# Performance work log

Measured on AMD Instinct MI355X. Metric: run time of the kernel, lower is better.

The kernel has to match this reference:

```python
import jax, jax.numpy as jnp
import numpy as np

B, N, E, H = 2, 4096, 512, 8
D = E // H  # head size


def setup_inputs() -> dict:
    key = jax.random.key(0)
    ks = jax.random.split(key, 11)
    s = 1.0 / np.sqrt(E)
    inp = {
        'q': jax.random.normal(ks[0], (B, N, E), jnp.float32),
        'k': jax.random.normal(ks[1], (B, N, E), jnp.float32),
        'v': jax.random.normal(ks[2], (B, N, E), jnp.float32),
        'Wq': jax.random.uniform(ks[3], (E, E), jnp.float32, -s, s),
        'bq': jax.random.uniform(ks[4], (E,), jnp.float32, -s, s),
        'Wk': jax.random.uniform(ks[5], (E, E), jnp.float32, -s, s),
        'bk': jax.random.uniform(ks[6], (E,), jnp.float32, -s, s),
        'Wv': jax.random.uniform(ks[7], (E, E), jnp.float32, -s, s),
        'bv': jax.random.uniform(ks[8], (E,), jnp.float32, -s, s),
        'Wo': jax.random.uniform(ks[9], (E, E), jnp.float32, -s, s),
        'bo': jax.random.uniform(ks[10], (E,), jnp.float32, -s, s),
    }
    return inp


def reference(q, k, v, Wq, bq, Wk, bk, Wv, bv, Wo, bo):
    # Linear projections (torch Linear: x @ W.T + b)
    qp = (q @ Wq.T + bq).reshape(B, N, H, D).transpose(0, 2, 1, 3)  # [B,H,N,D]
    kp = (k @ Wk.T + bk).reshape(B, N, H, D).transpose(0, 2, 1, 3)
    vp = (v @ Wv.T + bv).reshape(B, N, H, D).transpose(0, 2, 1, 3)
    scores = jnp.einsum('bhnd,bhmd->bhnm', qp, kp) / jnp.sqrt(jnp.float32(D))
    attn = jax.nn.softmax(scores, axis=-1)
    out = jnp.einsum('bhnm,bhmd->bhnd', attn, vp)  # [B,H,N,D]
    out = out.transpose(0, 2, 1, 3).reshape(B, N, E)
    return out @ Wo.T + bo
```

## Files before the change

### kernel.cpp

```cpp
#include <hip/hip_runtime.h>
#include <hip/hip_bf16.h>
#include <cstddef>
#include <cstdint>


typedef __bf16 bf16_t;
typedef __bf16 bf16x8 __attribute__((ext_vector_type(8)));
typedef __bf16 bf16x4 __attribute__((ext_vector_type(4)));
typedef float  f32x4  __attribute__((ext_vector_type(4)));

#define MFMA_BF16 __builtin_amdgcn_mfma_f32_16x16x32_bf16

static __device__ __forceinline__ bf16x8 cvt2(const float4& a, const float4& b) {
  return bf16x8{(bf16_t)a.x,(bf16_t)a.y,(bf16_t)a.z,(bf16_t)a.w,
                (bf16_t)b.x,(bf16_t)b.y,(bf16_t)b.z,(bf16_t)b.w};
}

static __device__ __forceinline__ uint32_t pk2(float a, float b) {
  uint32_t r;
  asm("v_cvt_pk_bf16_f32 %0, %1, %2" : "=v"(r) : "v"(a), "v"(b));
  return r;
}

__global__ void __launch_bounds__(256, 2)
qkv_proj(const float* __restrict__ q, const float* __restrict__ k,
         const float* __restrict__ v,
         const float* __restrict__ Wq, const float* __restrict__ bq,
         const float* __restrict__ Wk, const float* __restrict__ bk,
         const float* __restrict__ Wv, const float* __restrict__ bv,
         bf16_t* __restrict__ Qp, bf16_t* __restrict__ Kp,
         bf16_t* __restrict__ Vt, float qscale)
{
  __shared__ __align__(16) bf16_t As[2][128 * 72];
  __shared__ __align__(16) bf16_t Bs[2][128 * 72];
  const int l     = blockIdx.x;
  const int slice = l >> 8;
  const int inner = l & 255;
  const int mtile = ((inner >> 5) << 3) | (inner & 7);
  const int ntile = (inner >> 3) & 3;
  const int tid   = threadIdx.x;
  const int w     = tid >> 6;
  const int lane  = tid & 63;
  const int lr    = lane & 15;
  const int quad  = lane >> 4;
  const int wm    = w & 1;
  const int wn    = w >> 1;
  const int xrow  = tid >> 1, xcol = (tid & 1) << 5;

  const float* Xf   = (slice == 0) ? q  : (slice == 1) ? k  : v;
  const float* W    = (slice == 0) ? Wq : (slice == 1) ? Wk : Wv;
  const float* bias = (slice == 0) ? bq : (slice == 1) ? bk : bv;
  const float scale = (slice == 0) ? qscale : 1.0f;

  float bvv[4];
#pragma unroll
  for (int ci = 0; ci < 4; ++ci) bvv[ci] = bias[ntile * 128 + wn * 64 + ci * 16 + lr];

  f32x4 acc[4][4] = {};
  float4 xa[8], wa[8];

#pragma unroll
  for (int j = 0; j < 4; ++j) {
    const float* p = Xf + (size_t)(mtile * 128 + xrow) * 512 + xcol + j * 8;
    xa[2*j]   = *(const float4*)p;
    xa[2*j+1] = *(const float4*)(p + 4);
    const float* pw = W + (size_t)(ntile * 128 + xrow) * 512 + xcol + j * 8;
    wa[2*j]   = *(const float4*)pw;
    wa[2*j+1] = *(const float4*)(pw + 4);
  }
#pragma unroll
  for (int j = 0; j < 4; ++j) {
    *(bf16x8*)(&As[0][xrow * 72 + xcol + j * 8]) = cvt2(xa[2*j], xa[2*j+1]);
    *(bf16x8*)(&Bs[0][xrow * 72 + xcol + j * 8]) = cvt2(wa[2*j], wa[2*j+1]);
  }
  __syncthreads();

  for (int it = 0; it < 8; ++it) {
    const int cur = it & 1, nxt = cur ^ 1;
    if (it != 7) {
      const int k0 = (it + 1) << 6;
#pragma unroll
      for (int j = 0; j < 4; ++j) {
        const float* p = Xf + (size_t)(mtile * 128 + xrow) * 512 + k0 + xcol + j * 8;
        xa[2*j]   = *(const float4*)p;
        xa[2*j+1] = *(const float4*)(p + 4);
        const float* pw = W + (size_t)(ntile * 128 + xrow) * 512 + k0 + xcol + j * 8;
        wa[2*j]   = *(const float4*)pw;
        wa[2*j+1] = *(const float4*)(pw + 4);
      }
    }
    bf16x8 af[4][2], bfr[4][2];
#pragma unroll
    for (int mi = 0; mi < 4; ++mi)
#pragma unroll
      for (int kh = 0; kh < 2; ++kh)
        af[mi][kh] = *(const bf16x8*)(&As[cur][(wm * 64 + mi * 16 + lr) * 72 + (kh * 4 + quad) * 8]);
#pragma unroll
    for (int ci = 0; ci < 4; ++ci)
#pragma unroll
      for (int kh = 0; kh < 2; ++kh)
        bfr[ci][kh] = *(const bf16x8*)(&Bs[cur][(wn * 64 + ci * 16 + lr) * 72 + (kh * 4 + quad) * 8]);
#pragma unroll
    for (int mi = 0; mi < 4; ++mi)
#pragma unroll
      for (int ci = 0; ci < 4; ++ci) {
        acc[mi][ci] = MFMA_BF16(af[mi][0], bfr[ci][0], acc[mi][ci], 0, 0, 0);
        acc[mi][ci] = MFMA_BF16(af[mi][1], bfr[ci][1], acc[mi][ci], 0, 0, 0);
      }
    if (it != 7) {
#pragma unroll
      for (int j = 0; j < 4; ++j) {
        *(bf16x8*)(&As[nxt][xrow * 72 + xcol + j * 8]) = cvt2(xa[2*j], xa[2*j+1]);
        *(bf16x8*)(&Bs[nxt][xrow * 72 + xcol + j * 8]) = cvt2(wa[2*j], wa[2*j+1]);
      }
    }
    __syncthreads();
  }

  bf16_t* outQK = (slice == 0) ? Qp : Kp;
#pragma unroll
  for (int mi = 0; mi < 4; ++mi) {
    const int gm0 = mtile * 128 + wm * 64 + mi * 16 + quad * 4;
#pragma unroll
    for (int ci = 0; ci < 4; ++ci) {
      const int gc = ntile * 128 + wn * 64 + ci * 16 + lr;
      const int h = gc >> 6, dd = gc & 63;
      if (slice < 2) {
#pragma unroll
        for (int r = 0; r < 4; ++r) {
          const int gm = gm0 + r;
          const int b = gm >> 12, n = gm & 4095;
          outQK[(size_t)((b * 8 + h) * 4096 + n) * 64 + dd] =
              (bf16_t)((acc[mi][ci][r] + bvv[ci]) * scale);
        }
      } else {
        const int b = gm0 >> 12, n0 = gm0 & 4095;
        bf16x4 pk;
#pragma unroll
        for (int r = 0; r < 4; ++r) pk[r] = (bf16_t)(acc[mi][ci][r] + bvv[ci]);
        *(bf16x4*)(Vt + (size_t)((b * 8 + h) * 64 + dd) * 4096 + n0) = pk;
      }
    }
  }
}

__global__ void __launch_bounds__(256, 2)
o_proj(const bf16_t* __restrict__ Xb, const float* __restrict__ W,
       const float* __restrict__ bias, float* __restrict__ out)
{
  __shared__ __align__(16) bf16_t As[2][128 * 72];
  __shared__ __align__(16) bf16_t Bs[2][128 * 72];
  const int l     = blockIdx.x;
  const int mtile = ((l >> 5) << 3) | (l & 7);
  const int ntile = (l >> 3) & 3;
  const int tid   = threadIdx.x;
  const int w     = tid >> 6;
  const int lane  = tid & 63;
  const int lr    = lane & 15;
  const int quad  = lane >> 4;
  const int wm    = w & 1;
  const int wn    = w >> 1;
  const int xrow  = tid >> 1, xcol = (tid & 1) << 5;

  float bvv[4];
#pragma unroll
  for (int ci = 0; ci < 4; ++ci) bvv[ci] = bias[ntile * 128 + wn * 64 + ci * 16 + lr];

  f32x4 acc[4][4] = {};
  float4 wa[8];
  bf16x8 xb[4];

#pragma unroll
  for (int j = 0; j < 4; ++j) {
    xb[j] = *(const bf16x8*)(Xb + (size_t)(mtile * 128 + xrow) * 512 + xcol + j * 8);
    const float* pw = W + (size_t)(ntile * 128 + xrow) * 512 + xcol + j * 8;
    wa[2*j]   = *(const float4*)pw;
    wa[2*j+1] = *(const float4*)(pw + 4);
  }
#pragma unroll
  for (int j = 0; j < 4; ++j) {
    *(bf16x8*)(&As[0][xrow * 72 + xcol + j * 8]) = xb[j];
    *(bf16x8*)(&Bs[0][xrow * 72 + xcol + j * 8]) = cvt2(wa[2*j], wa[2*j+1]);
  }
  __syncthreads();

  for (int it = 0; it < 8; ++it) {
    const int cur = it & 1, nxt = cur ^ 1;
    if (it != 7) {
      const int k0 = (it + 1) << 6;
#pragma unroll
      for (int j = 0; j < 4; ++j) {
        xb[j] = *(const bf16x8*)(Xb + (size_t)(mtile * 128 + xrow) * 512 + k0 + xcol + j * 8);
        const float* pw = W + (size_t)(ntile * 128 + xrow) * 512 + k0 + xcol + j * 8;
        wa[2*j]   = *(const float4*)pw;
        wa[2*j+1] = *(const float4*)(pw + 4);
      }
    }
    bf16x8 af[4][2], bfr[4][2];
#pragma unroll
    for (int mi = 0; mi < 4; ++mi)
#pragma unroll
      for (int kh = 0; kh < 2; ++kh)
        af[mi][kh] = *(const bf16x8*)(&As[cur][(wm * 64 + mi * 16 + lr) * 72 + (kh * 4 + quad) * 8]);
#pragma unroll
    for (int ci = 0; ci < 4; ++ci)
#pragma unroll
      for (int kh = 0; kh < 2; ++kh)
        bfr[ci][kh] = *(const bf16x8*)(&Bs[cur][(wn * 64 + ci * 16 + lr) * 72 + (kh * 4 + quad) * 8]);
#pragma unroll
    for (int mi = 0; mi < 4; ++mi)
#pragma unroll
      for (int ci = 0; ci < 4; ++ci) {
        acc[mi][ci] = MFMA_BF16(af[mi][0], bfr[ci][0], acc[mi][ci], 0, 0, 0);
        acc[mi][ci] = MFMA_BF16(af[mi][1], bfr[ci][1], acc[mi][ci], 0, 0, 0);
      }
    if (it != 7) {
#pragma unroll
      for (int j = 0; j < 4; ++j) {
        *(bf16x8*)(&As[nxt][xrow * 72 + xcol + j * 8]) = xb[j];
        *(bf16x8*)(&Bs[nxt][xrow * 72 + xcol + j * 8]) = cvt2(wa[2*j], wa[2*j+1]);
      }
    }
    __syncthreads();
  }

#pragma unroll
  for (int mi = 0; mi < 4; ++mi) {
    const int gm0 = mtile * 128 + wm * 64 + mi * 16 + quad * 4;
#pragma unroll
    for (int ci = 0; ci < 4; ++ci) {
      const int gc = ntile * 128 + wn * 64 + ci * 16 + lr;
#pragma unroll
      for (int r = 0; r < 4; ++r)
        out[(size_t)(gm0 + r) * 512 + gc] = acc[mi][ci][r] + bvv[ci];
    }
  }
}

__global__ void __launch_bounds__(256, 2)
flash_attn(const bf16_t* __restrict__ Qp, const bf16_t* __restrict__ Kp,
           const bf16_t* __restrict__ Vt, bf16_t* __restrict__ Oc)
{
  __shared__ __align__(16) bf16_t Klds[2][64 * 72];
  __shared__ __align__(16) bf16_t Vlds[2][64 * 72];

  const int tid  = threadIdx.x;
  const int w    = tid >> 6;
  const int lane = tid & 63, lr = lane & 15, quad = lane >> 4;
  const int bh   = blockIdx.x;
  const int qt0  = blockIdx.y * 128 + w * 32;

  const bf16_t* Qh = Qp + (size_t)bh * 4096 * 64;
  const bf16_t* Kh = Kp + (size_t)bh * 4096 * 64;
  const bf16_t* Vh = Vt + (size_t)bh * 64 * 4096;

  const int srow = w * 16 + (lane >> 2);
  const int scol = (lane & 3) << 4;

  bf16x8 qf[2][2];
#pragma unroll
  for (int qi = 0; qi < 2; ++qi)
#pragma unroll
    for (int kh = 0; kh < 2; ++kh)
      qf[qi][kh] = *(const bf16x8*)(Qh + (size_t)(qt0 + qi * 16 + lr) * 64 + kh * 32 + quad * 8);

  bf16x8 kst[2], vst[2];
#pragma unroll
  for (int j = 0; j < 2; ++j) {
    kst[j] = *(const bf16x8*)(Kh + (size_t)srow * 64 + scol + j * 8);
    vst[j] = *(const bf16x8*)(Vh + (size_t)srow * 4096 + scol + j * 8);
  }
#pragma unroll
  for (int j = 0; j < 2; ++j) {
    *(bf16x8*)(&Klds[0][srow * 72 + scol + j * 8]) = kst[j];
    *(bf16x8*)(&Vlds[0][srow * 72 + scol + j * 8]) = vst[j];
  }
  __syncthreads();

  f32x4 acc[2][4] = {};
  float lsum[2] = {0.f, 0.f};
  const f32x4 zero = {0.f, 0.f, 0.f, 0.f};

  for (int it = 0; it < 64; ++it) {
    const int cur = it & 1, nxt = cur ^ 1;

    if (it != 63) {
      const int kvn = (it + 1) << 6;
#pragma unroll
      for (int j = 0; j < 2; ++j) {
        kst[j] = *(const bf16x8*)(Kh + (size_t)(kvn + srow) * 64 + scol + j * 8);
        vst[j] = *(const bf16x8*)(Vh + (size_t)srow * 4096 + kvn + scol + j * 8);
      }
    }

    bf16x8 kf[4][2];
#pragma unroll
    for (int mt = 0; mt < 4; ++mt)
#pragma unroll
      for (int kh = 0; kh < 2; ++kh)
        kf[mt][kh] = *(const bf16x8*)(&Klds[cur][(mt * 16 + lr) * 72 + (kh * 4 + quad) * 8]);
    bf16x8 vf[4][2];
#pragma unroll
    for (int t = 0; t < 4; ++t)
#pragma unroll
      for (int kvh = 0; kvh < 2; ++kvh)
        vf[t][kvh] = *(const bf16x8*)(&Vlds[cur][(t * 16 + lr) * 72 + (kvh * 4 + quad) * 8]);

    f32x4 sT[4][2];
#pragma unroll
    for (int mt = 0; mt < 4; ++mt)
#pragma unroll
      for (int qi = 0; qi < 2; ++qi) {
        sT[mt][qi] = MFMA_BF16(kf[mt][0], qf[qi][0], zero, 0, 0, 0);
        sT[mt][qi] = MFMA_BF16(kf[mt][1], qf[qi][1], sT[mt][qi], 0, 0, 0);
      }

    bf16x8 pa[2][2];
#pragma unroll
    for (int qi = 0; qi < 2; ++qi) {
      uint32_t ap[4], bp[4];
#pragma unroll
      for (int mt = 0; mt < 4; ++mt) {
        float p0 = __builtin_amdgcn_exp2f(sT[mt][qi][0]);
        float p1 = __builtin_amdgcn_exp2f(sT[mt][qi][1]);
        float p2 = __builtin_amdgcn_exp2f(sT[mt][qi][2]);
        float p3 = __builtin_amdgcn_exp2f(sT[mt][qi][3]);
        lsum[qi] += (p0 + p1) + (p2 + p3);
        ap[mt] = pk2(p0, p1);
        bp[mt] = pk2(p2, p3);
      }
#pragma unroll
      for (int kvh = 0; kvh < 2; ++kvh) {
        uint32_t xa_ = ap[2 * kvh], ya_ = ap[2 * kvh + 1];
        asm("v_permlane32_swap_b32 %0, %1" : "+v"(xa_), "+v"(ya_));
        asm("v_permlane16_swap_b32 %0, %1" : "+v"(xa_), "+v"(ya_));
        uint32_t xb_ = bp[2 * kvh], yb_ = bp[2 * kvh + 1];
        asm("v_permlane32_swap_b32 %0, %1" : "+v"(xb_), "+v"(yb_));
        asm("v_permlane16_swap_b32 %0, %1" : "+v"(xb_), "+v"(yb_));
        union { uint32_t u[4]; bf16x8 v; } pu;
        pu.u[0] = xa_; pu.u[1] = xb_; pu.u[2] = ya_; pu.u[3] = yb_;
        pa[qi][kvh] = pu.v;
      }
    }

#pragma unroll
    for (int t = 0; t < 4; ++t)
#pragma unroll
      for (int qi = 0; qi < 2; ++qi) {
        acc[qi][t] = MFMA_BF16(pa[qi][0], vf[t][0], acc[qi][t], 0, 0, 0);
        acc[qi][t] = MFMA_BF16(pa[qi][1], vf[t][1], acc[qi][t], 0, 0, 0);
      }

    if (it != 63) {
#pragma unroll
      for (int j = 0; j < 2; ++j) {
        *(bf16x8*)(&Klds[nxt][srow * 72 + scol + j * 8]) = kst[j];
        *(bf16x8*)(&Vlds[nxt][srow * 72 + scol + j * 8]) = vst[j];
      }
    }
    __syncthreads();
  }

#pragma unroll
  for (int qi = 0; qi < 2; ++qi) {
    lsum[qi] += __shfl_xor(lsum[qi], 16);
    lsum[qi] += __shfl_xor(lsum[qi], 32);
  }

  const int b = bh >> 3, h = bh & 7;
  bf16_t* Ob = Oc + (size_t)b * 4096 * 512 + h * 64;
#pragma unroll
  for (int qi = 0; qi < 2; ++qi) {
    float inv[4];
#pragma unroll
    for (int r = 0; r < 4; ++r)
      inv[r] = 1.0f / __shfl(lsum[qi], quad * 4 + r);
#pragma unroll
    for (int t = 0; t < 4; ++t)
#pragma unroll
      for (int r = 0; r < 4; ++r) {
        const int n = qt0 + qi * 16 + quad * 4 + r;
        Ob[(size_t)n * 512 + t * 16 + lr] = (bf16_t)(acc[qi][t][r] * inv[r]);
      }
  }
}

extern "C" void kernel_launch(void* const* d_in, const int* in_sizes, int n_in,
                              void* d_out, int out_size, void* d_ws, size_t ws_size,
                              hipStream_t stream)
{
  const float* q  = (const float*)d_in[0];
  const float* k  = (const float*)d_in[1];
  const float* v  = (const float*)d_in[2];
  const float* Wq = (const float*)d_in[3];
  const float* bq = (const float*)d_in[4];
  const float* Wk = (const float*)d_in[5];
  const float* bk = (const float*)d_in[6];
  const float* Wv = (const float*)d_in[7];
  const float* bv = (const float*)d_in[8];
  const float* Wo = (const float*)d_in[9];
  const float* bo = (const float*)d_in[10];

  const size_t HEAD_ELEMS = (size_t)2 * 8 * 4096 * 64;
  bf16_t* Qp = (bf16_t*)d_ws;
  bf16_t* Kp = Qp + HEAD_ELEMS;
  bf16_t* Vt = Kp + HEAD_ELEMS;
  bf16_t* Oc = Vt + HEAD_ELEMS;

  const float qscale = 0.125f * 1.44269504f;

  qkv_proj<<<dim3(768), 256, 0, stream>>>(q, k, v, Wq, bq, Wk, bk, Wv, bv,
                                          Qp, Kp, Vt, qscale);
  flash_attn<<<dim3(16, 32), 256, 0, stream>>>(Qp, Kp, Vt, Oc);
  o_proj<<<dim3(256), 256, 0, stream>>>(Oc, Wo, bo, (float*)d_out);
}
```

Baseline: 260.6 us.

## Pre-convert inputs and weights to bf16 and retile output projection

Adds a separate conversion kernel that turns q/k/v and all four weight matrices into bf16 in workspace, so the projection GEMMs load half-width bf16 tiles with no in-loop conversion. The output projection is retiled to 128x64 tiles with twice as many blocks, raising parallelism. The cost is an extra kernel launch plus a full fp32 read and bf16 write of the inputs. Oc now reuses the qb buffer.

```diff
diff --git a/kernel.cpp b/kernel.cpp
--- a/kernel.cpp
+++ b/kernel.cpp
@@ -22,12 +22,48 @@
   return r;
 }
 
+__global__ void __launch_bounds__(256)
+cvt_bf16(const float* __restrict__ q, const float* __restrict__ k,
+         const float* __restrict__ v, const float* __restrict__ Wq,
+         const float* __restrict__ Wk, const float* __restrict__ Wv,
+         const float* __restrict__ Wo,
+         bf16_t* __restrict__ qb, bf16_t* __restrict__ kb,
+         bf16_t* __restrict__ vb, bf16_t* __restrict__ wq,
+         bf16_t* __restrict__ wk, bf16_t* __restrict__ wv,
+         bf16_t* __restrict__ wo)
+{
+  const int CQ = 524288;
+  const int CW = 32768;
+  const int TOT = 3 * CQ + 4 * CW;
+  const int STRIDE = 2048 * 256;
+  for (int c = blockIdx.x * 256 + threadIdx.x; c < TOT; c += STRIDE) {
+    const float* src; bf16_t* dst; int off;
+    if (c < 3 * CQ) {
+      const int t = c >> 19;
+      const int r = c & (CQ - 1);
+      src = (t == 0) ? q : (t == 1) ? k : v;
+      dst = (t == 0) ? qb : (t == 1) ? kb : vb;
+      off = r << 3;
+    } else {
+      const int c2 = c - 3 * CQ;
+      const int t = c2 >> 15;
+      const int r = c2 & (CW - 1);
+      src = (t == 0) ? Wq : (t == 1) ? Wk : (t == 2) ? Wv : Wo;
+      dst = (t == 0) ? wq : (t == 1) ? wk : (t == 2) ? wv : wo;
+      off = r << 3;
+    }
+    const float4 a = *(const float4*)(src + off);
+    const float4 b = *(const float4*)(src + off + 4);
+    *(bf16x8*)(dst + off) = cvt2(a, b);
+  }
+}
+
 __global__ void __launch_bounds__(256, 2)
-qkv_proj(const float* __restrict__ q, const float* __restrict__ k,
-         const float* __restrict__ v,
-         const float* __restrict__ Wq, const float* __restrict__ bq,
-         const float* __restrict__ Wk, const float* __restrict__ bk,
-         const float* __restrict__ Wv, const float* __restrict__ bv,
+qkv_proj(const bf16_t* __restrict__ qb, const bf16_t* __restrict__ kb,
+         const bf16_t* __restrict__ vb,
+         const bf16_t* __restrict__ Wqb, const float* __restrict__ bq,
+         const bf16_t* __restrict__ Wkb, const float* __restrict__ bk,
+         const bf16_t* __restrict__ Wvb, const float* __restrict__ bv,
          bf16_t* __restrict__ Qp, bf16_t* __restrict__ Kp,
          bf16_t* __restrict__ Vt, float qscale)
 {
@@ -47,31 +83,27 @@
   const int wn    = w >> 1;
   const int xrow  = tid >> 1, xcol = (tid & 1) << 5;
 
-  const float* Xf   = (slice == 0) ? q  : (slice == 1) ? k  : v;
-  const float* W    = (slice == 0) ? Wq : (slice == 1) ? Wk : Wv;
-  const float* bias = (slice == 0) ? bq : (slice == 1) ? bk : bv;
-  const float scale = (slice == 0) ? qscale : 1.0f;
+  const bf16_t* Xb   = (slice == 0) ? qb  : (slice == 1) ? kb  : vb;
+  const bf16_t* W    = (slice == 0) ? Wqb : (slice == 1) ? Wkb : Wvb;
+  const float*  bias = (slice == 0) ? bq  : (slice == 1) ? bk  : bv;
+  const float scale  = (slice == 0) ? qscale : 1.0f;
 
   float bvv[4];
 #pragma unroll
   for (int ci = 0; ci < 4; ++ci) bvv[ci] = bias[ntile * 128 + wn * 64 + ci * 16 + lr];
 
   f32x4 acc[4][4] = {};
-  float4 xa[8], wa[8];
+  bf16x8 xa[4], wa[4];
 
 #pragma unroll
   for (int j = 0; j < 4; ++j) {
-    const float* p = Xf + (size_t)(mtile * 128 + xrow) * 512 + xcol + j * 8;
-    xa[2*j]   = *(const float4*)p;
-    xa[2*j+1] = *(const float4*)(p + 4);
-    const float* pw = W + (size_t)(ntile * 128 + xrow) * 512 + xcol + j * 8;
-    wa[2*j]   = *(const float4*)pw;
-    wa[2*j+1] = *(const float4*)(pw + 4);
+    xa[j] = *(const bf16x8*)(Xb + (size_t)(mtile * 128 + xrow) * 512 + xcol + j * 8);
+    wa[j] = *(const bf16x8*)(W  + (size_t)(ntile * 128 + xrow) * 512 + xcol + j * 8);
   }
 #pragma unroll
   for (int j = 0; j < 4; ++j) {
-    *(bf16x8*)(&As[0][xrow * 72 + xcol + j * 8]) = cvt2(xa[2*j], xa[2*j+1]);
-    *(bf16x8*)(&Bs[0][xrow * 72 + xcol + j * 8]) = cvt2(wa[2*j], wa[2*j+1]);
+    *(bf16x8*)(&As[0][xrow * 72 + xcol + j * 8]) = xa[j];
+    *(bf16x8*)(&Bs[0][xrow * 72 + xcol + j * 8]) = wa[j];
   }
   __syncthreads();
 
@@ -81,12 +113,8 @@
       const int k0 = (it + 1) << 6;
 #pragma unroll
       for (int j = 0; j < 4; ++j) {
-        const float* p = Xf + (size_t)(mtile * 128 + xrow) * 512 + k0 + xcol + j * 8;
-        xa[2*j]   = *(const float4*)p;
-        xa[2*j+1] = *(const float4*)(p + 4);
-        const float* pw = W + (size_t)(ntile * 128 + xrow) * 512 + k0 + xcol + j * 8;
-        wa[2*j]   = *(const float4*)pw;
-        wa[2*j+1] = *(const float4*)(pw + 4);
+        xa[j] = *(const bf16x8*)(Xb + (size_t)(mtile * 128 + xrow) * 512 + k0 + xcol + j * 8);
+        wa[j] = *(const bf16x8*)(W  + (size_t)(ntile * 128 + xrow) * 512 + k0 + xcol + j * 8);
       }
     }
     bf16x8 af[4][2], bfr[4][2];
@@ -110,8 +138,8 @@
     if (it != 7) {
 #pragma unroll
       for (int j = 0; j < 4; ++j) {
-        *(bf16x8*)(&As[nxt][xrow * 72 + xcol + j * 8]) = cvt2(xa[2*j], xa[2*j+1]);
-        *(bf16x8*)(&Bs[nxt][xrow * 72 + xcol + j * 8]) = cvt2(wa[2*j], wa[2*j+1]);
+        *(bf16x8*)(&As[nxt][xrow * 72 + xcol + j * 8]) = xa[j];
+        *(bf16x8*)(&Bs[nxt][xrow * 72 + xcol + j * 8]) = wa[j];
       }
     }
     __syncthreads();
@@ -145,14 +173,14 @@
 }
 
 __global__ void __launch_bounds__(256, 2)
-o_proj(const bf16_t* __restrict__ Xb, const float* __restrict__ W,
+o_proj(const bf16_t* __restrict__ Xb, const bf16_t* __restrict__ W,
        const float* __restrict__ bias, float* __restrict__ out)
 {
   __shared__ __align__(16) bf16_t As[2][128 * 72];
-  __shared__ __align__(16) bf16_t Bs[2][128 * 72];
+  __shared__ __align__(16) bf16_t Bs[2][64 * 72];
   const int l     = blockIdx.x;
-  const int mtile = ((l >> 5) << 3) | (l & 7);
-  const int ntile = (l >> 3) & 3;
+  const int mtile = ((l >> 6) << 3) | (l & 7);
+  const int ntile = (l >> 3) & 7;
   const int tid   = threadIdx.x;
   const int w     = tid >> 6;
   const int lane  = tid & 63;
@@ -161,27 +189,27 @@
   const int wm    = w & 1;
   const int wn    = w >> 1;
   const int xrow  = tid >> 1, xcol = (tid & 1) << 5;
-
-  float bvv[4];
-#pragma unroll
-  for (int ci = 0; ci < 4; ++ci) bvv[ci] = bias[ntile * 128 + wn * 64 + ci * 16 + lr];
-
-  f32x4 acc[4][4] = {};
-  float4 wa[8];
-  bf16x8 xb[4];
-
-#pragma unroll
-  for (int j = 0; j < 4; ++j) {
+  const int wrow  = tid >> 2, wcol = (tid & 3) << 4;
+
+  float bvv[2];
+#pragma unroll
+  for (int ci = 0; ci < 2; ++ci) bvv[ci] = bias[ntile * 64 + wn * 32 + ci * 16 + lr];
+
+  f32x4 acc[4][2] = {};
+  bf16x8 xb[4], wb[2];
+
+#pragma unroll
+  for (int j = 0; j < 4; ++j)
     xb[j] = *(const bf16x8*)(Xb + (size_t)(mtile * 128 + xrow) * 512 + xcol + j * 8);
-    const float* pw = W + (size_t)(ntile * 128 + xrow) * 512 + xcol + j * 8;
-    wa[2*j]   = *(const float4*)pw;
-    wa[2*j+1] = *(const float4*)(pw + 4);
-  }
-#pragma unroll
-  for (int j = 0; j < 4; ++j) {
+#pragma unroll
+  for (int j = 0; j < 2; ++j)
+    wb[j] = *(const bf16x8*)(W + (size_t)(ntile * 64 + wrow) * 512 + wcol + j * 8);
+#pragma unroll
+  for (int j = 0; j < 4; ++j)
     *(bf16x8*)(&As[0][xrow * 72 + xcol + j * 8]) = xb[j];
-    *(bf16x8*)(&Bs[0][xrow * 72 + xcol + j * 8]) = cvt2(wa[2*j], wa[2*j+1]);
-  }
+#pragma unroll
+  for (int j = 0; j < 2; ++j)
+    *(bf16x8*)(&Bs[0][wrow * 72 + wcol + j * 8]) = wb[j];
   __syncthreads();
 
   for (int it = 0; it < 8; ++it) {
@@ -189,37 +217,37 @@
     if (it != 7) {
       const int k0 = (it + 1) << 6;
 #pragma unroll
-      for (int j = 0; j < 4; ++j) {
+      for (int j = 0; j < 4; ++j)
         xb[j] = *(const bf16x8*)(Xb + (size_t)(mtile * 128 + xrow) * 512 + k0 + xcol + j * 8);
-        const float* pw = W + (size_t)(ntile * 128 + xrow) * 512 + k0 + xcol + j * 8;
-        wa[2*j]   = *(const float4*)pw;
-        wa[2*j+1] = *(const float4*)(pw + 4);
-      }
-    }
-    bf16x8 af[4][2], bfr[4][2];
+#pragma unroll
+      for (int j = 0; j < 2; ++j)
+        wb[j] = *(const bf16x8*)(W + (size_t)(ntile * 64 + wrow) * 512 + k0 + wcol + j * 8);
+    }
+    bf16x8 af[4][2], bfr[2][2];
 #pragma unroll
     for (int mi = 0; mi < 4; ++mi)
 #pragma unroll
       for (int kh = 0; kh < 2; ++kh)
         af[mi][kh] = *(const bf16x8*)(&As[cur][(wm * 64 + mi * 16 + lr) * 72 + (kh * 4 + quad) * 8]);
 #pragma unroll
-    for (int ci = 0; ci < 4; ++ci)
+    for (int ci = 0; ci < 2; ++ci)
 #pragma unroll
       for (int kh = 0; kh < 2; ++kh)
-        bfr[ci][kh] = *(const bf16x8*)(&Bs[cur][(wn * 64 + ci * 16 + lr) * 72 + (kh * 4 + quad) * 8]);
+        bfr[ci][kh] = *(const bf16x8*)(&Bs[cur][(wn * 32 + ci * 16 + lr) * 72 + (kh * 4 + quad) * 8]);
 #pragma unroll
     for (int mi = 0; mi < 4; ++mi)
 #pragma unroll
-      for (int ci = 0; ci < 4; ++ci) {
+      for (int ci = 0; ci < 2; ++ci) {
         acc[mi][ci] = MFMA_BF16(af[mi][0], bfr[ci][0], acc[mi][ci], 0, 0, 0);
         acc[mi][ci] = MFMA_BF16(af[mi][1], bfr[ci][1], acc[mi][ci], 0, 0, 0);
       }
     if (it != 7) {
 #pragma unroll
-      for (int j = 0; j < 4; ++j) {
+      for (int j = 0; j < 4; ++j)
         *(bf16x8*)(&As[nxt][xrow * 72 + xcol + j * 8]) = xb[j];
-        *(bf16x8*)(&Bs[nxt][xrow * 72 + xcol + j * 8]) = cvt2(wa[2*j], wa[2*j+1]);
-      }
+#pragma unroll
+      for (int j = 0; j < 2; ++j)
+        *(bf16x8*)(&Bs[nxt][wrow * 72 + wcol + j * 8]) = wb[j];
     }
     __syncthreads();
   }
@@ -228,8 +256,8 @@
   for (int mi = 0; mi < 4; ++mi) {
     const int gm0 = mtile * 128 + wm * 64 + mi * 16 + quad * 4;
 #pragma unroll
-    for (int ci = 0; ci < 4; ++ci) {
-      const int gc = ntile * 128 + wn * 64 + ci * 16 + lr;
+    for (int ci = 0; ci < 2; ++ci) {
+      const int gc = ntile * 64 + wn * 32 + ci * 16 + lr;
 #pragma unroll
       for (int r = 0; r < 4; ++r)
         out[(size_t)(gm0 + r) * 512 + gc] = acc[mi][ci][r] + bvv[ci];
@@ -402,15 +430,27 @@
   const float* bo = (const float*)d_in[10];
 
   const size_t HEAD_ELEMS = (size_t)2 * 8 * 4096 * 64;
-  bf16_t* Qp = (bf16_t*)d_ws;
-  bf16_t* Kp = Qp + HEAD_ELEMS;
-  bf16_t* Vt = Kp + HEAD_ELEMS;
-  bf16_t* Oc = Vt + HEAD_ELEMS;
+  const size_t W_ELEMS    = (size_t)512 * 512;
+
+  bf16_t* base = (bf16_t*)d_ws;
+  bf16_t* qb  = base;
+  bf16_t* kb  = qb + HEAD_ELEMS;
+  bf16_t* vb  = kb + HEAD_ELEMS;
+  bf16_t* Qp  = vb + HEAD_ELEMS;
+  bf16_t* Kp  = Qp + HEAD_ELEMS;
+  bf16_t* Vt  = Kp + HEAD_ELEMS;
+  bf16_t* wqb = Vt + HEAD_ELEMS;
+  bf16_t* wkb = wqb + W_ELEMS;
+  bf16_t* wvb = wkb + W_ELEMS;
+  bf16_t* wob = wvb + W_ELEMS;
+  bf16_t* Oc  = qb;
 
   const float qscale = 0.125f * 1.44269504f;
 
-  qkv_proj<<<dim3(768), 256, 0, stream>>>(q, k, v, Wq, bq, Wk, bk, Wv, bv,
-                                          Qp, Kp, Vt, qscale);
+  cvt_bf16<<<dim3(2048), 256, 0, stream>>>(q, k, v, Wq, Wk, Wv, Wo,
+                                           qb, kb, vb, wqb, wkb, wvb, wob);
+  qkv_proj<<<dim3(768), 256, 0, stream>>>(qb, kb, vb, wqb, bq, wkb, bk,
+                                          wvb, bv, Qp, Kp, Vt, qscale);
   flash_attn<<<dim3(16, 32), 256, 0, stream>>>(Qp, Kp, Vt, Oc);
-  o_proj<<<dim3(256), 256, 0, stream>>>(Oc, Wo, bo, (float*)d_out);
-}
+  o_proj<<<dim3(512), 256, 0, stream>>>(Oc, wob, bo, (float*)d_out);
+}
```

Result: faster. 225.0 us (-13.6%).
